# Kernel tuning notes

Hardware: AMD Instinct MI355X
Metric: run time of the kernel (lower is better)

## Reference

```python
import jax, jax.numpy as jnp
import numpy as np

H, KV, D, HID, Q, S = 16, 8, 128, 2048, 1024, 8192
CACHE_POS = 4096

def rotate_half(x, axis):
    x1, x2 = jnp.split(x, 2, axis)
    return jnp.concatenate((-x2, x1), axis=axis)

def setup_inputs() -> dict:
    key = jax.random.key(0)
    ks = jax.random.split(key, 12)
    hidden_states = jax.random.normal(ks[0], (1, HID, 1, Q), jnp.float32)
    # RoPE tables for the new token positions [CACHE_POS, CACHE_POS+Q)
    pos = jnp.arange(CACHE_POS, CACHE_POS + Q, dtype=jnp.float32)
    inv_freq = 1.0 / (10000.0 ** (jnp.arange(0, D, 2, dtype=jnp.float32) / D))
    ang = pos[:, None] * inv_freq[None, :]                      # (Q, D/2)
    cos = jnp.tile(jnp.cos(ang), (1, 2))[None, None]            # (1,1,Q,D)
    sin = jnp.tile(jnp.sin(ang), (1, 2))[None, None]
    cos_t = jnp.transpose(cos, (0, 1, 3, 2))                    # (1,1,D,Q)
    sin_t = jnp.transpose(sin, (0, 1, 3, 2))
    # causal mask over full cache: key slot s visible to query i iff s <= CACHE_POS + i
    k_idx = jnp.arange(S)[:, None]
    q_idx = jnp.arange(Q)[None, :]
    attention_mask = jnp.where(k_idx <= CACHE_POS + q_idx, 0.0, -1e9).astype(jnp.float32)[None, None]  # (1,1,S,Q)
    key_cache = 0.02 * jax.random.normal(ks[1], (1, KV, S, D), jnp.float32)
    value_cache = 0.02 * jax.random.normal(ks[2], (1, KV, S, D), jnp.float32)
    w = lambda k, shp: 0.02 * jax.random.normal(k, shp, jnp.float32)
    return dict(hidden_states=hidden_states, cos=cos, sin=sin, cos_t=cos_t, sin_t=sin_t,
                attention_mask=attention_mask, key_cache=key_cache, value_cache=value_cache,
                Wq=w(ks[3], (HID, HID)), bq=w(ks[4], (HID,)),
                Wk=w(ks[5], (KV * D, HID)), bk=w(ks[6], (KV * D,)),
                Wv=w(ks[7], (KV * D, HID)), bv=w(ks[8], (KV * D,)),
                Wo=w(ks[9], (HID, HID)), cache_position=CACHE_POS)

def reference(hidden_states, cos, sin, cos_t, sin_t, attention_mask,
              key_cache, value_cache, Wq, bq, Wk, bk, Wv, bv, Wo, cache_position):
    # 1x1-conv style projections on channels-first (1, C, 1, Q)
    q = jnp.einsum('oc,bcxq->boxq', Wq, hidden_states) + bq[None, :, None, None]
    k = jnp.einsum('oc,bcxq->boxq', Wk, hidden_states) + bk[None, :, None, None]
    v = jnp.einsum('oc,bcxq->boxq', Wv, hidden_states) + bv[None, :, None, None]
    q = q.reshape(1, H, D, Q)                                   # (1,H,D,Q)
    k = k.reshape(1, KV, D, Q).transpose(0, 1, 3, 2)            # (1,KV,Q,D)
    v = v.reshape(1, KV, D, Q).transpose(0, 1, 3, 2)
    # inline RoPE: q along head_dim axis (-2), k along last axis
    q = q * cos_t + rotate_half(q, -2) * sin_t
    k = k * cos + rotate_half(k, -1) * sin
    # KV-cache scatter at layer_idx=0, offset cache_position
    key_cache = jax.lax.dynamic_update_slice(key_cache, k, (0, 0, cache_position, 0))
    value_cache = jax.lax.dynamic_update_slice(value_cache, v, (0, 0, cache_position, 0))
    k_all = key_cache[0]                                        # (KV,S,D)
    v_all = value_cache[0]
    qg = q.reshape(KV, H // KV, D, Q)                           # GQA groups
    scores = jnp.einsum('ksd,kgdq->kgsq', k_all, qg) / jnp.sqrt(jnp.float32(D))
    scores = scores + attention_mask[0]                         # (1,S,Q) broadcast
    w = jax.nn.softmax(scores, axis=2)                          # softmax over cache slots
    out = jnp.einsum('kgsq,ksd->kgdq', w, v_all)                # (KV,G,D,Q)
    out = out.reshape(1, H * D, 1, Q)
    attn_output = jnp.einsum('oc,bcxq->boxq', Wo, out)
    return attn_output
```

## Files before the change

kernel.cpp:

```cpp
#include <hip/hip_runtime.h>

#define H_HEADS 16
#define KV_HEADS 8
#define DHEAD 128
#define HID 2048
#define NQ 1024
#define SCACHE 8192
#define CPOS 4096
#define SEFF 5120

typedef __attribute__((ext_vector_type(8))) __bf16 bf16x8;
typedef __attribute__((ext_vector_type(4))) float f32x4;
typedef unsigned short u16;
typedef unsigned int u32;

__device__ __forceinline__ u16 f2b(float f) {
  u32 u = __float_as_uint(f);
  u += 0x7fffu + ((u >> 16) & 1u);
  return (u16)(u >> 16);
}
__device__ __forceinline__ u16 f2b_t(float f) {
  return (u16)(__float_as_uint(f) >> 16);
}
__device__ __forceinline__ float b2f(u16 b) { return __uint_as_float(((u32)b) << 16); }
__device__ __forceinline__ u32 pk2(u16 a, u16 b) { return (u32)a | ((u32)b << 16); }
__device__ __forceinline__ uint2 f4b4(float4 v) {
  uint2 o;
  o.x = pk2(f2b(v.x), f2b(v.y));
  o.y = pk2(f2b(v.z), f2b(v.w));
  return o;
}

union U4 { uint4 v; u16 u[8]; };

__global__ void __launch_bounds__(256) k_conv_w(const float* __restrict__ Wq,
                                                const float* __restrict__ Wk,
                                                const float* __restrict__ Wv,
                                                u16* __restrict__ Wb) {
  int i = blockIdx.x * 256 + threadIdx.x;
  const float* src;
  int off;
  if (i < 1048576) { src = Wq; off = i; }
  else if (i < 1572864) { src = Wk; off = i - 1048576; }
  else { src = Wv; off = i - 1572864; }
  float4 v = ((const float4*)src)[off];
  *(uint2*)(Wb + (size_t)i * 4) = f4b4(v);
}

__global__ void __launch_bounds__(256) k_f32_to_bf16(const float* __restrict__ src,
                                                     u16* __restrict__ dst, int n4) {
  int i = blockIdx.x * 256 + threadIdx.x;
  if (i < n4) {
    float4 v = ((const float4*)src)[i];
    *(uint2*)(dst + (size_t)i * 4) = f4b4(v);
  }
}

__global__ void __launch_bounds__(256) k_transpose_h(const float* __restrict__ hid,
                                                     u16* __restrict__ hT) {
  __shared__ __align__(16) float ls[64 * 68];
  int t = threadIdx.x;
  int c0 = blockIdx.x * 64, q0 = blockIdx.y * 64;
#pragma unroll
  for (int it = 0; it < 4; ++it) {
    int c = it * 256 + t;
    int row = c >> 4, ch = c & 15;
    *(float4*)(ls + row * 68 + ch * 4) =
        *(const float4*)(hid + (size_t)(c0 + row) * NQ + q0 + ch * 4);
  }
  __syncthreads();
  int ql = t & 63, cch = t >> 6;
  u32 ob[8];
#pragma unroll
  for (int j = 0; j < 8; ++j)
    ob[j] = pk2(f2b(ls[(cch * 16 + 2 * j) * 68 + ql]), f2b(ls[(cch * 16 + 2 * j + 1) * 68 + ql]));
  uint4* dst = (uint4*)(hT + (size_t)(q0 + ql) * HID + c0 + cch * 16);
  dst[0] = make_uint4(ob[0], ob[1], ob[2], ob[3]);
  dst[1] = make_uint4(ob[4], ob[5], ob[6], ob[7]);
}

__global__ void __launch_bounds__(256) k_prep_vT(const float* __restrict__ vc,
                                                 u16* __restrict__ vT) {
  __shared__ __align__(16) float ls[64 * 132];
  int t = threadIdx.x;
  int s0 = blockIdx.x * 64;
  int kv = blockIdx.y;
#pragma unroll
  for (int it = 0; it < 8; ++it) {
    int c = it * 256 + t;
    int row = c >> 5, ch = c & 31;
    *(float4*)(ls + row * 132 + ch * 4) =
        *(const float4*)(vc + ((size_t)kv * SCACHE + s0 + row) * DHEAD + ch * 4);
  }
  __syncthreads();
  int d = t >> 1, sch = t & 1;
  u32 ob[16];
#pragma unroll
  for (int j = 0; j < 16; ++j)
    ob[j] = pk2(f2b(ls[(sch * 32 + 2 * j) * 132 + d]), f2b(ls[(sch * 32 + 2 * j + 1) * 132 + d]));
  uint4* dst = (uint4*)(vT + ((size_t)kv * DHEAD + d) * SEFF + s0 + sch * 32);
#pragma unroll
  for (int j = 0; j < 4; ++j)
    dst[j] = make_uint4(ob[4 * j], ob[4 * j + 1], ob[4 * j + 2], ob[4 * j + 3]);
}

__global__ void __launch_bounds__(256) k_conv_k(const float* __restrict__ kc,
                                                u16* __restrict__ kb) {
  int i = blockIdx.x * 256 + threadIdx.x;
  int kvi = i >> 17;
  int rem = i & 131071;
  float4 v = *(const float4*)(kc + (size_t)kvi * SCACHE * DHEAD + (size_t)rem * 4);
  *(uint2*)(kb + (size_t)kvi * SEFF * DHEAD + (size_t)rem * 4) = f4b4(v);
}

__global__ void __launch_bounds__(256) k_copy_vnew(const u16* __restrict__ qkv,
                                                   u16* __restrict__ vT) {
  int i = blockIdx.x * 256 + threadIdx.x;
  int row = i >> 7, ch = i & 127;
  *(uint4*)(vT + (size_t)row * SEFF + CPOS + ch * 8) =
      *(const uint4*)(qkv + (size_t)(3072 + row) * NQ + ch * 8);
}

__global__ void __launch_bounds__(256) k_rope_t(const u16* __restrict__ qkv,
                                                const float* __restrict__ cosb,
                                                const float* __restrict__ sinb,
                                                u16* __restrict__ qb,
                                                u16* __restrict__ kb) {
  __shared__ __align__(16) u16 ls[64 * 136];
  int t = threadIdx.x;
  int hh = blockIdx.x;
  int q0 = blockIdx.y * 64;
  bool isq = hh < 16;
  int rowbase = isq ? hh * DHEAD : HID + (hh - 16) * DHEAD;
#pragma unroll
  for (int it = 0; it < 4; ++it) {
    int c = it * 256 + t;
    int d = c >> 3, qc = (c & 7) * 8;
    U4 v;
    v.v = *(const uint4*)(qkv + (size_t)(rowbase + d) * NQ + q0 + qc);
#pragma unroll
    for (int e = 0; e < 8; ++e) ls[(qc + e) * 136 + d] = v.u[e];
  }
  __syncthreads();
  int ql = t & 63, hf = t >> 6;
  int q = q0 + ql;
  float scale = isq ? 0.08838834764831845f : 1.0f;
  u16* dst = isq ? (qb + ((size_t)hh * NQ + q) * DHEAD)
                 : (kb + ((size_t)(hh - 16) * SEFF + CPOS + q) * DHEAD);
#pragma unroll
  for (int g = 0; g < 4; ++g) {
    int d0 = hf * 32 + g * 8;
    U4 x, y;
    x.v = *(uint4*)(ls + ql * 136 + d0);
    y.v = *(uint4*)(ls + ql * 136 + (d0 ^ 64));
    float4 ca = *(const float4*)(cosb + (size_t)q * DHEAD + d0);
    float4 cb = *(const float4*)(cosb + (size_t)q * DHEAD + d0 + 4);
    float4 sa = *(const float4*)(sinb + (size_t)q * DHEAD + d0);
    float4 sb = *(const float4*)(sinb + (size_t)q * DHEAD + d0 + 4);
    float cs[8] = {ca.x, ca.y, ca.z, ca.w, cb.x, cb.y, cb.z, cb.w};
    float sn[8] = {sa.x, sa.y, sa.z, sa.w, sb.x, sb.y, sb.z, sb.w};
    float sgn = (d0 < 64) ? -1.0f : 1.0f;
    u32 ob[4];
#pragma unroll
    for (int e = 0; e < 4; ++e) {
      float r0 = (b2f(x.u[2 * e]) * cs[2 * e] + sgn * b2f(y.u[2 * e]) * sn[2 * e]) * scale;
      float r1 = (b2f(x.u[2 * e + 1]) * cs[2 * e + 1] + sgn * b2f(y.u[2 * e + 1]) * sn[2 * e + 1]) * scale;
      ob[e] = pk2(f2b(r0), f2b(r1));
    }
    *(uint4*)(dst + d0) = make_uint4(ob[0], ob[1], ob[2], ob[3]);
  }
}

__global__ void __launch_bounds__(256) k_gemm_qkv(
    const u16* __restrict__ Wb, const u16* __restrict__ hT, u16* __restrict__ qkv,
    const float* __restrict__ bq, const float* __restrict__ bk, const float* __restrict__ bv) {
  __shared__ __align__(16) u16 lsA[128 * 32];
  __shared__ __align__(16) u16 lsB[128 * 32];
  int t = threadIdx.x;
  int m0 = blockIdx.x * 128, n0 = blockIdx.y * 128;
  const u16* Abase = Wb + (size_t)m0 * HID;
  int lane = t & 63, wid = t >> 6;
  int quad = lane >> 4, l15 = lane & 15;
  int wr = wid >> 1, wc = wid & 1;
  f32x4 acc[4][4];
#pragma unroll
  for (int i = 0; i < 4; ++i)
#pragma unroll
    for (int j = 0; j < 4; ++j) acc[i][j] = (f32x4){0.f, 0.f, 0.f, 0.f};
  for (int kt = 0; kt < HID; kt += 32) {
    __syncthreads();
#pragma unroll
    for (int it = 0; it < 2; ++it) {
      int c = it * 256 + t;
      int row = c >> 2, ch = c & 3;
      *(uint4*)(lsA + row * 32 + ch * 8) =
          *(const uint4*)(Abase + (size_t)row * HID + kt + ch * 8);
      *(uint4*)(lsB + row * 32 + ch * 8) =
          *(const uint4*)(hT + (size_t)(n0 + row) * HID + kt + ch * 8);
    }
    __syncthreads();
    bf16x8 af[4], bfr[4];
#pragma unroll
    for (int i = 0; i < 4; ++i)
      af[i] = *(const bf16x8*)(lsA + (wr * 64 + i * 16 + l15) * 32 + quad * 8);
#pragma unroll
    for (int j = 0; j < 4; ++j)
      bfr[j] = *(const bf16x8*)(lsB + (wc * 64 + j * 16 + l15) * 32 + quad * 8);
#pragma unroll
    for (int i = 0; i < 4; ++i)
#pragma unroll
      for (int j = 0; j < 4; ++j)
        acc[i][j] = __builtin_amdgcn_mfma_f32_16x16x32_bf16(af[i], bfr[j], acc[i][j], 0, 0, 0);
  }
#pragma unroll
  for (int i = 0; i < 4; ++i) {
#pragma unroll
    for (int r = 0; r < 4; ++r) {
      int m = m0 + wr * 64 + i * 16 + quad * 4 + r;
      float bias = (m < 2048) ? bq[m] : ((m < 3072) ? bk[m - 2048] : bv[m - 3072]);
#pragma unroll
      for (int j = 0; j < 4; ++j) {
        int n = n0 + wc * 64 + j * 16 + l15;
        qkv[(size_t)m * NQ + n] = f2b(acc[i][j][r] + bias);
      }
    }
  }
}

__global__ void __launch_bounds__(512) k_flash(const u16* __restrict__ qb,
                                               const u16* __restrict__ kb,
                                               const u16* __restrict__ vT,
                                               u16* __restrict__ po,
                                               float* __restrict__ pm,
                                               float* __restrict__ pl) {
  __shared__ __align__(16) u16 lsK[64 * 136];
  __shared__ __align__(16) u16 lsV[128 * 72];
  __shared__ __align__(16) u16 lsP[8 * 16 * 72];
  int t = threadIdx.x;
  int h = blockIdx.x, qt = blockIdx.y, z = blockIdx.z;
  int kv = h >> 1;
  int q0 = qt * 128;
  int lane = t & 63, wid = t >> 6;
  int quad = lane >> 4, l15 = lane & 15;
  int qw = q0 + wid * 16;

  union { u16 u[8]; bf16x8 v; } onesu;
#pragma unroll
  for (int e = 0; e < 8; ++e) onesu.u[e] = 0x3f80;
  bf16x8 onesf = onesu.v;

  bf16x8 qf[4];
  const u16* qrow = qb + ((size_t)h * NQ + qw + l15) * DHEAD;
#pragma unroll
  for (int kc = 0; kc < 4; ++kc) qf[kc] = *(const bf16x8*)(qrow + kc * 32 + quad * 8);
  f32x4 oacc[8];
#pragma unroll
  for (int f = 0; f < 8; ++f) oacc[f] = (f32x4){0.f, 0.f, 0.f, 0.f};
  f32x4 lacc = (f32x4){0.f, 0.f, 0.f, 0.f};
  float m_run[4];
#pragma unroll
  for (int r = 0; r < 4; ++r) m_run[r] = -1e30f;
  u16* lsPw = lsP + wid * (16 * 72);
  int Svis = CPOS + q0 + 128;
  const u16* kbase = kb + (size_t)kv * SEFF * DHEAD;
  const u16* vbase = vT + (size_t)kv * DHEAD * SEFF;

  int rK = t >> 4, cK = (t & 15) * 8;
  int rV = t >> 3, cV = (t & 7) * 8;
  uint4 pk0, pk1, pv0, pv1;
  {
    int s0 = z * 64;
    pk0 = *(const uint4*)(kbase + (size_t)(s0 + rK) * DHEAD + cK);
    pk1 = *(const uint4*)(kbase + (size_t)(s0 + 32 + rK) * DHEAD + cK);
    pv0 = *(const uint4*)(vbase + (size_t)rV * SEFF + s0 + cV);
    pv1 = *(const uint4*)(vbase + (size_t)(64 + rV) * SEFF + s0 + cV);
  }
  for (int s0 = z * 64; s0 < Svis; s0 += 256) {
    __syncthreads();
    *(uint4*)(lsK + rK * 136 + cK) = pk0;
    *(uint4*)(lsK + (32 + rK) * 136 + cK) = pk1;
    *(uint4*)(lsV + rV * 72 + cV) = pv0;
    *(uint4*)(lsV + (64 + rV) * 72 + cV) = pv1;
    __syncthreads();
    int sn = s0 + 256;
    if (sn < Svis) {
      pk0 = *(const uint4*)(kbase + (size_t)(sn + rK) * DHEAD + cK);
      pk1 = *(const uint4*)(kbase + (size_t)(sn + 32 + rK) * DHEAD + cK);
      pv0 = *(const uint4*)(vbase + (size_t)rV * SEFF + sn + cV);
      pv1 = *(const uint4*)(vbase + (size_t)(64 + rV) * SEFF + sn + cV);
    }
    f32x4 sc[4];
#pragma unroll
    for (int js = 0; js < 4; ++js) {
      sc[js] = (f32x4){0.f, 0.f, 0.f, 0.f};
#pragma unroll
      for (int kc = 0; kc < 4; ++kc) {
        bf16x8 kf = *(const bf16x8*)(lsK + (js * 16 + l15) * 136 + kc * 32 + quad * 8);
        sc[js] = __builtin_amdgcn_mfma_f32_16x16x32_bf16(qf[kc], kf, sc[js], 0, 0, 0);
      }
    }
    if (s0 + 63 > CPOS + qw) {
#pragma unroll
      for (int r = 0; r < 4; ++r) {
        int lim = CPOS + qw + quad * 4 + r - s0;
#pragma unroll
        for (int js = 0; js < 4; ++js) {
          bool valid = (js * 16 + l15) <= lim;
          sc[js][r] = valid ? sc[js][r] : -1e30f;
        }
      }
    }
    float alpha[4];
#pragma unroll
    for (int r = 0; r < 4; ++r) {
      float mx = fmaxf(fmaxf(sc[0][r], sc[1][r]), fmaxf(sc[2][r], sc[3][r]));
      mx = fmaxf(mx, __shfl_xor(mx, 1, 64));
      mx = fmaxf(mx, __shfl_xor(mx, 2, 64));
      mx = fmaxf(mx, __shfl_xor(mx, 4, 64));
      mx = fmaxf(mx, __shfl_xor(mx, 8, 64));
      float mnew = fmaxf(m_run[r], mx);
      alpha[r] = __expf(m_run[r] - mnew);
      m_run[r] = mnew;
#pragma unroll
      for (int js = 0; js < 4; ++js) {
        float p = __expf(sc[js][r] - mnew);
        lsPw[(quad * 4 + r) * 72 + js * 16 + l15] = f2b_t(p);
      }
    }
#pragma unroll
    for (int f = 0; f < 8; ++f)
#pragma unroll
      for (int r = 0; r < 4; ++r) oacc[f][r] *= alpha[r];
#pragma unroll
    for (int r = 0; r < 4; ++r) lacc[r] *= alpha[r];
    bf16x8 pf[2];
#pragma unroll
    for (int ks = 0; ks < 2; ++ks)
      pf[ks] = *(const bf16x8*)(lsPw + l15 * 72 + ks * 32 + quad * 8);
#pragma unroll
    for (int f = 0; f < 8; ++f) {
#pragma unroll
      for (int ks = 0; ks < 2; ++ks) {
        bf16x8 vf = *(const bf16x8*)(lsV + (f * 16 + l15) * 72 + ks * 32 + quad * 8);
        oacc[f] = __builtin_amdgcn_mfma_f32_16x16x32_bf16(pf[ks], vf, oacc[f], 0, 0, 0);
      }
    }
#pragma unroll
    for (int ks = 0; ks < 2; ++ks)
      lacc = __builtin_amdgcn_mfma_f32_16x16x32_bf16(pf[ks], onesf, lacc, 0, 0, 0);
  }
  int p = (h * 8 + qt) * 4 + z;
#pragma unroll
  for (int r = 0; r < 4; ++r) {
    int qloc = wid * 16 + quad * 4 + r;
    if (l15 == 0) {
      pm[(size_t)p * 128 + qloc] = m_run[r];
      pl[(size_t)p * 128 + qloc] = lacc[r];
    }
#pragma unroll
    for (int f = 0; f < 8; ++f)
      po[(size_t)p * 16384 + qloc * 128 + f * 16 + l15] = f2b(oacc[f][r]);
  }
}

__global__ void __launch_bounds__(256) k_combine(const u16* __restrict__ po,
                                                 const float* __restrict__ pm,
                                                 const float* __restrict__ pl,
                                                 u16* __restrict__ outT) {
  int t = threadIdx.x;
  int h = blockIdx.x, qt = blockIdx.y;
  int q = qt * 64 + (t >> 2);
  int dq = (t & 3) * 32;
  int pb = (h * 8 + (q >> 7)) * 4;
  int ql = q & 127;
  float m0 = pm[(size_t)(pb + 0) * 128 + ql];
  float m1 = pm[(size_t)(pb + 1) * 128 + ql];
  float m2 = pm[(size_t)(pb + 2) * 128 + ql];
  float m3 = pm[(size_t)(pb + 3) * 128 + ql];
  float M = fmaxf(fmaxf(m0, m1), fmaxf(m2, m3));
  float w[4] = {__expf(m0 - M), __expf(m1 - M), __expf(m2 - M), __expf(m3 - M)};
  float L = 0.f;
#pragma unroll
  for (int zz = 0; zz < 4; ++zz) L += w[zz] * pl[(size_t)(pb + zz) * 128 + ql];
  float acc[32];
#pragma unroll
  for (int e = 0; e < 32; ++e) acc[e] = 0.f;
#pragma unroll
  for (int zz = 0; zz < 4; ++zz) {
    const u16* src = po + (size_t)(pb + zz) * 16384 + ql * 128 + dq;
#pragma unroll
    for (int j = 0; j < 4; ++j) {
      U4 v;
      v.v = *(const uint4*)(src + j * 8);
#pragma unroll
      for (int e = 0; e < 8; ++e) acc[j * 8 + e] += w[zz] * b2f(v.u[e]);
    }
  }
  float inv = 1.0f / L;
  u16* dst = outT + (size_t)q * HID + h * DHEAD + dq;
#pragma unroll
  for (int j = 0; j < 4; ++j) {
    u32 ob[4];
#pragma unroll
    for (int e = 0; e < 4; ++e)
      ob[e] = pk2(f2b(acc[j * 8 + 2 * e] * inv), f2b(acc[j * 8 + 2 * e + 1] * inv));
    *(uint4*)(dst + j * 8) = make_uint4(ob[0], ob[1], ob[2], ob[3]);
  }
}

__global__ void __launch_bounds__(256) k_gemm_bt(const u16* __restrict__ A,
                                                 const u16* __restrict__ BT,
                                                 float* __restrict__ C) {
  __shared__ __align__(16) u16 lsA[128 * 32];
  __shared__ __align__(16) u16 lsB[64 * 32];
  int t = threadIdx.x;
  int m0 = blockIdx.x * 128, n0 = blockIdx.y * 64;
  const u16* Abase = A + (size_t)m0 * HID;
  const u16* Bbase = BT + (size_t)n0 * HID;
  int lane = t & 63, wid = t >> 6;
  int quad = lane >> 4, l15 = lane & 15;
  int wr = wid >> 1, wc = wid & 1;
  f32x4 acc[4][2];
#pragma unroll
  for (int i = 0; i < 4; ++i)
#pragma unroll
    for (int j = 0; j < 2; ++j) acc[i][j] = (f32x4){0.f, 0.f, 0.f, 0.f};
  for (int kt = 0; kt < HID; kt += 32) {
    __syncthreads();
#pragma unroll
    for (int it = 0; it < 2; ++it) {
      int c = it * 256 + t;
      int row = c >> 2, ch = c & 3;
      *(uint4*)(lsA + row * 32 + ch * 8) =
          *(const uint4*)(Abase + (size_t)row * HID + kt + ch * 8);
    }
    {
      int row = t >> 2, ch = t & 3;
      *(uint4*)(lsB + row * 32 + ch * 8) =
          *(const uint4*)(Bbase + (size_t)row * HID + kt + ch * 8);
    }
    __syncthreads();
    bf16x8 af[4], bfr[2];
#pragma unroll
    for (int i = 0; i < 4; ++i)
      af[i] = *(const bf16x8*)(lsA + (wr * 64 + i * 16 + l15) * 32 + quad * 8);
#pragma unroll
    for (int j = 0; j < 2; ++j)
      bfr[j] = *(const bf16x8*)(lsB + (wc * 32 + j * 16 + l15) * 32 + quad * 8);
#pragma unroll
    for (int i = 0; i < 4; ++i)
#pragma unroll
      for (int j = 0; j < 2; ++j)
        acc[i][j] = __builtin_amdgcn_mfma_f32_16x16x32_bf16(af[i], bfr[j], acc[i][j], 0, 0, 0);
  }
#pragma unroll
  for (int i = 0; i < 4; ++i)
#pragma unroll
    for (int r = 0; r < 4; ++r) {
      int m = m0 + wr * 64 + i * 16 + quad * 4 + r;
#pragma unroll
      for (int j = 0; j < 2; ++j) {
        int n = n0 + wc * 32 + j * 16 + l15;
        C[(size_t)m * NQ + n] = acc[i][j][r];
      }
    }
}

extern "C" void kernel_launch(void* const* d_in, const int* in_sizes, int n_in,
                              void* d_out, int out_size, void* d_ws, size_t ws_size,
                              hipStream_t stream) {
  (void)in_sizes; (void)n_in; (void)out_size; (void)ws_size;
  const float* hidden = (const float*)d_in[0];
  const float* cosb = (const float*)d_in[1];
  const float* sinb = (const float*)d_in[2];
  const float* kcache = (const float*)d_in[6];
  const float* vcache = (const float*)d_in[7];
  const float* Wq = (const float*)d_in[8];
  const float* bq = (const float*)d_in[9];
  const float* Wk = (const float*)d_in[10];
  const float* bk = (const float*)d_in[11];
  const float* Wv = (const float*)d_in[12];
  const float* bv = (const float*)d_in[13];
  const float* Wo = (const float*)d_in[14];

  char* ws = (char*)d_ws;
  u16* qkv = (u16*)(ws);
  u16* outT = (u16*)(ws + 8388608);
  u16* hT = outT;
  u16* vT = (u16*)(ws + 12582912);
  u16* Wob = vT;
  u16* kb = (u16*)(ws + 23068672);
  u16* qb = (u16*)(ws + 33554432);
  u16* Wb = (u16*)(ws + 12582912);
  u16* po = (u16*)(ws + 37748736);
  float* pm = (float*)(ws + 54525952);
  float* pl = (float*)(ws + 54788096);
  float* outb = (float*)d_out;

  k_conv_w<<<8192, 256, 0, stream>>>(Wq, Wk, Wv, Wb);
  k_transpose_h<<<dim3(32, 16), 256, 0, stream>>>(hidden, hT);
  k_gemm_qkv<<<dim3(32, 8), 256, 0, stream>>>(Wb, hT, qkv, bq, bk, bv);
  k_prep_vT<<<dim3(64, 8), 256, 0, stream>>>(vcache, vT);
  k_conv_k<<<4096, 256, 0, stream>>>(kcache, kb);
  k_rope_t<<<dim3(24, 16), 256, 0, stream>>>(qkv, cosb, sinb, qb, kb);
  k_copy_vnew<<<512, 256, 0, stream>>>(qkv, vT);
  k_flash<<<dim3(16, 8, 4), 512, 0, stream>>>(qb, kb, vT, po, pm, pl);
  k_f32_to_bf16<<<4096, 256, 0, stream>>>(Wo, Wob, 1048576);
  k_combine<<<dim3(16, 16), 256, 0, stream>>>(po, pm, pl, outT);
  k_gemm_bt<<<dim3(16, 16), 256, 0, stream>>>(Wob, outT, outb);
}
```

Baseline: 365.4 us.

## Double-buffer GEMM tiles with direct global-to-LDS loads and smaller tiles

Both the QKV projection GEMM and the output projection GEMM now stage A/B tiles into double-buffered LDS using global_load_lds, so the next K-slice is prefetched while MFMAs run on the current one. One barrier per iteration replaces two. The tiles also shrink (128x64 for QKV, 64x64 for the output GEMM), doubling the grid size to fill more CUs. The trade-off is lower per-block data reuse and more total global traffic.

```diff
diff --git a/kernel.cpp b/kernel.cpp
--- a/kernel.cpp
+++ b/kernel.cpp
@@ -29,6 +29,11 @@
   o.x = pk2(f2b(v.x), f2b(v.y));
   o.y = pk2(f2b(v.z), f2b(v.w));
   return o;
+}
+
+__device__ __forceinline__ void gld16(const u16* g, u16* l) {
+  __builtin_amdgcn_global_load_lds((const __attribute__((address_space(1))) void*)g,
+                                   (__attribute__((address_space(3))) void*)l, 16, 0, 0);
 }
 
 union U4 { uint4 v; u16 u[8]; };
@@ -174,43 +179,47 @@
 __global__ void __launch_bounds__(256) k_gemm_qkv(
     const u16* __restrict__ Wb, const u16* __restrict__ hT, u16* __restrict__ qkv,
     const float* __restrict__ bq, const float* __restrict__ bk, const float* __restrict__ bv) {
-  __shared__ __align__(16) u16 lsA[128 * 32];
-  __shared__ __align__(16) u16 lsB[128 * 32];
-  int t = threadIdx.x;
-  int m0 = blockIdx.x * 128, n0 = blockIdx.y * 128;
+  __shared__ __align__(16) u16 lsA[2][128 * 32];
+  __shared__ __align__(16) u16 lsB[2][64 * 32];
+  int t = threadIdx.x;
+  int m0 = blockIdx.x * 128, n0 = blockIdx.y * 64;
   const u16* Abase = Wb + (size_t)m0 * HID;
+  const u16* Bbase = hT + (size_t)n0 * HID;
   int lane = t & 63, wid = t >> 6;
   int quad = lane >> 4, l15 = lane & 15;
   int wr = wid >> 1, wc = wid & 1;
-  f32x4 acc[4][4];
+  int ra = t >> 2, ca = (t & 3) * 8;
+  f32x4 acc[4][2];
 #pragma unroll
   for (int i = 0; i < 4; ++i)
 #pragma unroll
-    for (int j = 0; j < 4; ++j) acc[i][j] = (f32x4){0.f, 0.f, 0.f, 0.f};
+    for (int j = 0; j < 2; ++j) acc[i][j] = (f32x4){0.f, 0.f, 0.f, 0.f};
+  gld16(Abase + (size_t)ra * HID + ca, lsA[0] + ra * 32 + ca);
+  gld16(Abase + (size_t)(64 + ra) * HID + ca, lsA[0] + (64 + ra) * 32 + ca);
+  gld16(Bbase + (size_t)ra * HID + ca, lsB[0] + ra * 32 + ca);
+  __syncthreads();
+  int cur = 0;
   for (int kt = 0; kt < HID; kt += 32) {
+    int kn = kt + 32;
+    if (kn < HID) {
+      gld16(Abase + (size_t)ra * HID + kn + ca, lsA[cur ^ 1] + ra * 32 + ca);
+      gld16(Abase + (size_t)(64 + ra) * HID + kn + ca, lsA[cur ^ 1] + (64 + ra) * 32 + ca);
+      gld16(Bbase + (size_t)ra * HID + kn + ca, lsB[cur ^ 1] + ra * 32 + ca);
+    }
+    bf16x8 af[4], bfr[2];
+#pragma unroll
+    for (int i = 0; i < 4; ++i)
+      af[i] = *(const bf16x8*)(lsA[cur] + (wr * 64 + i * 16 + l15) * 32 + quad * 8);
+#pragma unroll
+    for (int j = 0; j < 2; ++j)
+      bfr[j] = *(const bf16x8*)(lsB[cur] + (wc * 32 + j * 16 + l15) * 32 + quad * 8);
+#pragma unroll
+    for (int i = 0; i < 4; ++i)
+#pragma unroll
+      for (int j = 0; j < 2; ++j)
+        acc[i][j] = __builtin_amdgcn_mfma_f32_16x16x32_bf16(af[i], bfr[j], acc[i][j], 0, 0, 0);
     __syncthreads();
-#pragma unroll
-    for (int it = 0; it < 2; ++it) {
-      int c = it * 256 + t;
-      int row = c >> 2, ch = c & 3;
-      *(uint4*)(lsA + row * 32 + ch * 8) =
-          *(const uint4*)(Abase + (size_t)row * HID + kt + ch * 8);
-      *(uint4*)(lsB + row * 32 + ch * 8) =
-          *(const uint4*)(hT + (size_t)(n0 + row) * HID + kt + ch * 8);
-    }
-    __syncthreads();
-    bf16x8 af[4], bfr[4];
-#pragma unroll
-    for (int i = 0; i < 4; ++i)
-      af[i] = *(const bf16x8*)(lsA + (wr * 64 + i * 16 + l15) * 32 + quad * 8);
-#pragma unroll
-    for (int j = 0; j < 4; ++j)
-      bfr[j] = *(const bf16x8*)(lsB + (wc * 64 + j * 16 + l15) * 32 + quad * 8);
-#pragma unroll
-    for (int i = 0; i < 4; ++i)
-#pragma unroll
-      for (int j = 0; j < 4; ++j)
-        acc[i][j] = __builtin_amdgcn_mfma_f32_16x16x32_bf16(af[i], bfr[j], acc[i][j], 0, 0, 0);
+    cur ^= 1;
   }
 #pragma unroll
   for (int i = 0; i < 4; ++i) {
@@ -219,8 +228,8 @@
       int m = m0 + wr * 64 + i * 16 + quad * 4 + r;
       float bias = (m < 2048) ? bq[m] : ((m < 3072) ? bk[m - 2048] : bv[m - 3072]);
 #pragma unroll
-      for (int j = 0; j < 4; ++j) {
-        int n = n0 + wc * 64 + j * 16 + l15;
+      for (int j = 0; j < 2; ++j) {
+        int n = n0 + wc * 32 + j * 16 + l15;
         qkv[(size_t)m * NQ + n] = f2b(acc[i][j][r] + bias);
       }
     }
@@ -411,53 +420,51 @@
 __global__ void __launch_bounds__(256) k_gemm_bt(const u16* __restrict__ A,
                                                  const u16* __restrict__ BT,
                                                  float* __restrict__ C) {
-  __shared__ __align__(16) u16 lsA[128 * 32];
-  __shared__ __align__(16) u16 lsB[64 * 32];
-  int t = threadIdx.x;
-  int m0 = blockIdx.x * 128, n0 = blockIdx.y * 64;
+  __shared__ __align__(16) u16 lsA[2][64 * 32];
+  __shared__ __align__(16) u16 lsB[2][64 * 32];
+  int t = threadIdx.x;
+  int m0 = blockIdx.x * 64, n0 = blockIdx.y * 64;
   const u16* Abase = A + (size_t)m0 * HID;
   const u16* Bbase = BT + (size_t)n0 * HID;
   int lane = t & 63, wid = t >> 6;
   int quad = lane >> 4, l15 = lane & 15;
   int wr = wid >> 1, wc = wid & 1;
-  f32x4 acc[4][2];
-#pragma unroll
-  for (int i = 0; i < 4; ++i)
+  int ra = t >> 2, ca = (t & 3) * 8;
+  f32x4 acc[2][2];
+#pragma unroll
+  for (int i = 0; i < 2; ++i)
 #pragma unroll
     for (int j = 0; j < 2; ++j) acc[i][j] = (f32x4){0.f, 0.f, 0.f, 0.f};
+  gld16(Abase + (size_t)ra * HID + ca, lsA[0] + ra * 32 + ca);
+  gld16(Bbase + (size_t)ra * HID + ca, lsB[0] + ra * 32 + ca);
+  __syncthreads();
+  int cur = 0;
   for (int kt = 0; kt < HID; kt += 32) {
-    __syncthreads();
-#pragma unroll
-    for (int it = 0; it < 2; ++it) {
-      int c = it * 256 + t;
-      int row = c >> 2, ch = c & 3;
-      *(uint4*)(lsA + row * 32 + ch * 8) =
-          *(const uint4*)(Abase + (size_t)row * HID + kt + ch * 8);
-    }
-    {
-      int row = t >> 2, ch = t & 3;
-      *(uint4*)(lsB + row * 32 + ch * 8) =
-          *(const uint4*)(Bbase + (size_t)row * HID + kt + ch * 8);
-    }
-    __syncthreads();
-    bf16x8 af[4], bfr[2];
-#pragma unroll
-    for (int i = 0; i < 4; ++i)
-      af[i] = *(const bf16x8*)(lsA + (wr * 64 + i * 16 + l15) * 32 + quad * 8);
+    int kn = kt + 32;
+    if (kn < HID) {
+      gld16(Abase + (size_t)ra * HID + kn + ca, lsA[cur ^ 1] + ra * 32 + ca);
+      gld16(Bbase + (size_t)ra * HID + kn + ca, lsB[cur ^ 1] + ra * 32 + ca);
+    }
+    bf16x8 af[2], bfr[2];
+#pragma unroll
+    for (int i = 0; i < 2; ++i)
+      af[i] = *(const bf16x8*)(lsA[cur] + (wr * 32 + i * 16 + l15) * 32 + quad * 8);
 #pragma unroll
     for (int j = 0; j < 2; ++j)
-      bfr[j] = *(const bf16x8*)(lsB + (wc * 32 + j * 16 + l15) * 32 + quad * 8);
-#pragma unroll
-    for (int i = 0; i < 4; ++i)
+      bfr[j] = *(const bf16x8*)(lsB[cur] + (wc * 32 + j * 16 + l15) * 32 + quad * 8);
+#pragma unroll
+    for (int i = 0; i < 2; ++i)
 #pragma unroll
       for (int j = 0; j < 2; ++j)
         acc[i][j] = __builtin_amdgcn_mfma_f32_16x16x32_bf16(af[i], bfr[j], acc[i][j], 0, 0, 0);
-  }
-#pragma unroll
-  for (int i = 0; i < 4; ++i)
+    __syncthreads();
+    cur ^= 1;
+  }
+#pragma unroll
+  for (int i = 0; i < 2; ++i)
 #pragma unroll
     for (int r = 0; r < 4; ++r) {
-      int m = m0 + wr * 64 + i * 16 + quad * 4 + r;
+      int m = m0 + wr * 32 + i * 16 + quad * 4 + r;
 #pragma unroll
       for (int j = 0; j < 2; ++j) {
         int n = n0 + wc * 32 + j * 16 + l15;
@@ -499,7 +506,7 @@
 
   k_conv_w<<<8192, 256, 0, stream>>>(Wq, Wk, Wv, Wb);
   k_transpose_h<<<dim3(32, 16), 256, 0, stream>>>(hidden, hT);
-  k_gemm_qkv<<<dim3(32, 8), 256, 0, stream>>>(Wb, hT, qkv, bq, bk, bv);
+  k_gemm_qkv<<<dim3(32, 16), 256, 0, stream>>>(Wb, hT, qkv, bq, bk, bv);
   k_prep_vT<<<dim3(64, 8), 256, 0, stream>>>(vcache, vT);
   k_conv_k<<<4096, 256, 0, stream>>>(kcache, kb);
   k_rope_t<<<dim3(24, 16), 256, 0, stream>>>(qkv, cosb, sinb, qb, kb);
@@ -507,5 +514,5 @@
   k_flash<<<dim3(16, 8, 4), 512, 0, stream>>>(qb, kb, vT, po, pm, pl);
   k_f32_to_bf16<<<4096, 256, 0, stream>>>(Wo, Wob, 1048576);
   k_combine<<<dim3(16, 16), 256, 0, stream>>>(po, pm, pl, outT);
-  k_gemm_bt<<<dim3(16, 16), 256, 0, stream>>>(Wob, outT, outb);
-}
+  k_gemm_bt<<<dim3(32, 16), 256, 0, stream>>>(Wob, outT, outb);
+}
```

New measurement: 349.1 us. 4.4% less time.
